# Kernel optimization log

Hardware: AMD Instinct MI355X
Metric: run time of the kernel (lower is better)

The kernel has to match this reference:

```python
import jax, jax.numpy as jnp
import numpy as np

LN_EPS = 1e-5


def setup_inputs() -> dict:
    key = jax.random.key(0)
    ks = jax.random.split(key, 6)
    B, I, H = 16384, 512, 512
    x = jax.random.normal(ks[0], (B, I), dtype=jnp.float32)
    h_prev = jax.random.normal(ks[1], (B, H), dtype=jnp.float32)
    c_prev = jax.random.normal(ks[2], (B, H), dtype=jnp.float32)
    # packed gate weights in i|f|g|o order (equivalent to 8 separate matmuls)
    W_i = jax.random.normal(ks[3], (I, 4 * H), dtype=jnp.float32) * (1.0 / np.sqrt(I))
    W_h = jax.random.normal(ks[4], (H, 4 * H), dtype=jnp.float32) * (1.0 / np.sqrt(H))
    # biases: b_i=0, b_f=1, b_g=0, b_o=0 as in the torch module
    b = jnp.concatenate([jnp.zeros(H), jnp.ones(H), jnp.zeros(H), jnp.zeros(H)]).astype(jnp.float32)
    ln_weight = jnp.ones((H,), dtype=jnp.float32)
    ln_bias = jnp.zeros((H,), dtype=jnp.float32)
    return {"x": x, "h_prev": h_prev, "c_prev": c_prev, "W_i": W_i, "W_h": W_h,
            "b": b, "ln_weight": ln_weight, "ln_bias": ln_bias}


def layer_norm(h, w, bias):
    mu = jnp.mean(h, axis=-1, keepdims=True)
    var = jnp.var(h, axis=-1, keepdims=True)
    return (h - mu) * jax.lax.rsqrt(var + LN_EPS) * w + bias


def reference(x, h_prev, c_prev, W_i, W_h, b, ln_weight, ln_bias):
    H = h_prev.shape[-1]
    # two fused GEMMs covering all 4 gates: [B, 4H]
    gates = x @ W_i + h_prev @ W_h + b
    i, f, g, o = jnp.split(gates, 4, axis=-1)
    i = jax.nn.sigmoid(i)
    f = jax.nn.sigmoid(f)
    g = jnp.tanh(g)
    o = jax.nn.sigmoid(o)
    c = f * c_prev + i * g
    h = o * jnp.tanh(c)
    h = layer_norm(h, ln_weight, ln_bias)
    return (h, c)
```

## Files before the change

### kernel.cpp

```cpp
#include <hip/hip_runtime.h>
#include <cstdint>
#include <cstddef>

typedef unsigned short ushort_t;
typedef __attribute__((ext_vector_type(8))) short bf16x8;
typedef __attribute__((ext_vector_type(4))) float f32x4;

#define MROWS 16384
#define KDIM  1024
#define NDIM  2048
#define HDIM  512

static __device__ __forceinline__ unsigned short f2bf(float f) {
    unsigned int u = __float_as_uint(f);
    u += 0x7fffu + ((u >> 16) & 1u);
    return (unsigned short)(u >> 16);
}

static __device__ __forceinline__ float sigmoid_f(float x) {
    return 1.0f / (1.0f + __expf(-x));
}
static __device__ __forceinline__ float tanh_f(float x) {
    float t = __expf(2.0f * x);
    return 1.0f - 2.0f / (t + 1.0f);
}

__global__ __launch_bounds__(256) void pack_ab(const float* __restrict__ x,
                                               const float* __restrict__ hp,
                                               const float* __restrict__ Wi,
                                               const float* __restrict__ Wh,
                                               ushort_t* __restrict__ A,
                                               ushort_t* __restrict__ Bt) {
    __shared__ ushort_t sm[64][72];
    const int tid = threadIdx.x;
    if (blockIdx.x < 8192) {
        int t = blockIdx.x * 256 + tid;
        int row = t >> 7;
        int kc = (t & 127) << 3;
        const float* src = (kc < 512) ? (x + (size_t)row * 512 + kc)
                                      : (hp + (size_t)row * 512 + (kc - 512));
        float4 v0 = ((const float4*)src)[0];
        float4 v1 = ((const float4*)src)[1];
        ushort_t o[8] __attribute__((aligned(16)));
        o[0] = f2bf(v0.x); o[1] = f2bf(v0.y); o[2] = f2bf(v0.z); o[3] = f2bf(v0.w);
        o[4] = f2bf(v1.x); o[5] = f2bf(v1.y); o[6] = f2bf(v1.z); o[7] = f2bf(v1.w);
        *((uint4*)(A + (size_t)row * KDIM + kc)) = *((const uint4*)o);
    } else {
        int b2 = blockIdx.x - 8192;
        int kt = b2 >> 5;
        int ct = b2 & 31;
        const float* W = (kt < 8) ? (Wi + (size_t)(kt * 64) * NDIM)
                                  : (Wh + (size_t)((kt - 8) * 64) * NDIM);
        int c0 = (tid & 15) * 4;
        int r0 = tid >> 4;
#pragma unroll
        for (int r = 0; r < 4; ++r) {
            int krow = r * 16 + r0;
            float4 v = *((const float4*)(W + (size_t)krow * NDIM + ct * 64 + c0));
            sm[krow][c0 + 0] = f2bf(v.x);
            sm[krow][c0 + 1] = f2bf(v.y);
            sm[krow][c0 + 2] = f2bf(v.z);
            sm[krow][c0 + 3] = f2bf(v.w);
        }
        __syncthreads();
        int g = (ct * 64) >> 9;
        int h0 = ct * 64 - g * 512;
#pragma unroll
        for (int q = tid; q < 512; q += 256) {
            int cc = q >> 3;
            int kc = (q & 7) * 8;
            ushort_t o[8] __attribute__((aligned(16)));
#pragma unroll
            for (int j = 0; j < 8; ++j) o[j] = sm[kc + j][cc];
            int np = 4 * (h0 + cc) + g;
            *((uint4*)(Bt + (size_t)np * KDIM + kt * 64 + kc)) = *((const uint4*)o);
        }
    }
}

__global__ __launch_bounds__(256, 4) void gemm_cell(const ushort_t* __restrict__ A,
                                                    const ushort_t* __restrict__ Bt,
                                                    const float* __restrict__ b,
                                                    const float* __restrict__ c_prev,
                                                    float* __restrict__ h_out,
                                                    float* __restrict__ c_out) {
    __shared__ float smem_f[6144];
    ushort_t* Als = (ushort_t*)smem_f;
    ushort_t* Bls = Als + 128 * 64;

    const int tid  = threadIdx.x;
    const int w    = tid >> 6;
    const int lane = tid & 63;
    int bid = blockIdx.x;
    int lid = (bid >> 3) + (bid & 7) * 512;
    const int m0 = (lid >> 5) * 128;
    const int n0 = (lid & 31) * 64;
    const int wm = (w >> 1) * 64;
    const int wn = (w & 1) * 32;
    const int lr   = lane & 15;
    const int quad = lane >> 4;
    const int sw   = lr & 7;

    f32x4 zero = {0.f, 0.f, 0.f, 0.f};
    f32x4 acc[4][2];
#pragma unroll
    for (int i = 0; i < 4; ++i)
#pragma unroll
        for (int j = 0; j < 2; ++j) acc[i][j] = zero;

    for (int kt = 0; kt < KDIM / 64; ++kt) {
#pragma unroll
        for (int r = 0; r < 4; ++r) {
            int c = r * 256 + tid;
            int trow = c >> 3;
            int chg = (c & 7) ^ (trow & 7);
            const ushort_t* ga = A + (size_t)(m0 + trow) * KDIM + kt * 64 + chg * 8;
            __builtin_amdgcn_global_load_lds(
                (const __attribute__((address_space(1))) void*)ga,
                (__attribute__((address_space(3))) void*)((char*)Als + c * 16),
                16, 0, 0);
        }
#pragma unroll
        for (int r = 0; r < 2; ++r) {
            int c = r * 256 + tid;
            int trow = c >> 3;
            int chg = (c & 7) ^ (trow & 7);
            const ushort_t* gb = Bt + (size_t)(n0 + trow) * KDIM + kt * 64 + chg * 8;
            __builtin_amdgcn_global_load_lds(
                (const __attribute__((address_space(1))) void*)gb,
                (__attribute__((address_space(3))) void*)((char*)Bls + c * 16),
                16, 0, 0);
        }
        __syncthreads();

#pragma unroll
        for (int kk = 0; kk < 2; ++kk) {
            bf16x8 af[4], bf[2];
            int ch = kk * 4 + quad;
#pragma unroll
            for (int t2 = 0; t2 < 4; ++t2) {
                int ra = wm + t2 * 16 + lr;
                af[t2] = *((const bf16x8*)(Als + (ra * 8 + (ch ^ sw)) * 8));
            }
#pragma unroll
            for (int t2 = 0; t2 < 2; ++t2) {
                int rb = wn + t2 * 16 + lr;
                bf[t2] = *((const bf16x8*)(Bls + (rb * 8 + (ch ^ sw)) * 8));
            }
#pragma unroll
            for (int tm = 0; tm < 4; ++tm)
#pragma unroll
                for (int tn = 0; tn < 2; ++tn)
                    acc[tm][tn] = __builtin_amdgcn_mfma_f32_16x16x32_bf16(
                        af[tm], bf[tn], acc[tm][tn], 0, 0, 0);
        }
        __syncthreads();
    }

    float* scr = smem_f + w * 1024;
    const int hg0 = ((n0 + wn) >> 2) + ((lane & 1) << 2);
    const float4 bi4 = *((const float4*)(b + hg0));
    const float4 bf4 = *((const float4*)(b + 512 + hg0));
    const float4 bg4 = *((const float4*)(b + 1024 + hg0));
    const float4 bo4 = *((const float4*)(b + 1536 + hg0));
    const int rr = lane >> 1;

#pragma unroll
    for (int chunk = 0; chunk < 2; ++chunk) {
#pragma unroll
        for (int tm2 = 0; tm2 < 2; ++tm2) {
            int tm = chunk * 2 + tm2;
#pragma unroll
            for (int tn = 0; tn < 2; ++tn) {
                int c = tn * 16 + lr;
#pragma unroll
                for (int rg = 0; rg < 4; ++rg) {
                    int r = tm2 * 16 + quad * 4 + rg;
                    int blk = (c >> 2) ^ (r & 7);
                    scr[r * 32 + blk * 4 + (c & 3)] = acc[tm][tn][rg];
                }
            }
        }
        float4 gv[4];
#pragma unroll
        for (int j = 0; j < 4; ++j) {
            int hg_l = ((lane & 1) << 2) + j;
            int blk = hg_l ^ (rr & 7);
            gv[j] = *((const float4*)(scr + rr * 32 + blk * 4));
        }
        int grow = m0 + wm + chunk * 32 + rr;
        float4 cp = *((const float4*)(c_prev + (size_t)grow * HDIM + hg0));
        float cn[4], hv[4];
        {
            float iv, fv, g2, ov;
            iv = sigmoid_f(gv[0].x + bi4.x); fv = sigmoid_f(gv[0].y + bf4.x);
            g2 = tanh_f(gv[0].z + bg4.x);    ov = sigmoid_f(gv[0].w + bo4.x);
            cn[0] = fv * cp.x + iv * g2;     hv[0] = ov * tanh_f(cn[0]);
            iv = sigmoid_f(gv[1].x + bi4.y); fv = sigmoid_f(gv[1].y + bf4.y);
            g2 = tanh_f(gv[1].z + bg4.y);    ov = sigmoid_f(gv[1].w + bo4.y);
            cn[1] = fv * cp.y + iv * g2;     hv[1] = ov * tanh_f(cn[1]);
            iv = sigmoid_f(gv[2].x + bi4.z); fv = sigmoid_f(gv[2].y + bf4.z);
            g2 = tanh_f(gv[2].z + bg4.z);    ov = sigmoid_f(gv[2].w + bo4.z);
            cn[2] = fv * cp.z + iv * g2;     hv[2] = ov * tanh_f(cn[2]);
            iv = sigmoid_f(gv[3].x + bi4.w); fv = sigmoid_f(gv[3].y + bf4.w);
            g2 = tanh_f(gv[3].z + bg4.w);    ov = sigmoid_f(gv[3].w + bo4.w);
            cn[3] = fv * cp.w + iv * g2;     hv[3] = ov * tanh_f(cn[3]);
        }
        float4 cno = {cn[0], cn[1], cn[2], cn[3]};
        float4 hvo = {hv[0], hv[1], hv[2], hv[3]};
        *((float4*)(c_out + (size_t)grow * HDIM + hg0)) = cno;
        *((float4*)(h_out + (size_t)grow * HDIM + hg0)) = hvo;
    }
}

__global__ __launch_bounds__(256) void ln_kernel(float* __restrict__ h,
                                                 const float* __restrict__ lw,
                                                 const float* __restrict__ lb) {
    int w = threadIdx.x >> 6;
    int lane = threadIdx.x & 63;
    int row = blockIdx.x * 4 + w;
    float* p = h + (size_t)row * HDIM + lane * 8;
    float4 a = ((const float4*)p)[0];
    float4 c = ((const float4*)p)[1];
    float s  = a.x + a.y + a.z + a.w + c.x + c.y + c.z + c.w;
    float ss = a.x * a.x + a.y * a.y + a.z * a.z + a.w * a.w +
               c.x * c.x + c.y * c.y + c.z * c.z + c.w * c.w;
#pragma unroll
    for (int off = 32; off > 0; off >>= 1) {
        s  += __shfl_xor(s, off);
        ss += __shfl_xor(ss, off);
    }
    float mu = s * (1.0f / 512.0f);
    float var = ss * (1.0f / 512.0f) - mu * mu;
    float rstd = rsqrtf(var + 1e-5f);
    const float* wp = lw + lane * 8;
    const float* bp = lb + lane * 8;
    float4 w0 = ((const float4*)wp)[0];
    float4 w1 = ((const float4*)wp)[1];
    float4 b0 = ((const float4*)bp)[0];
    float4 b1 = ((const float4*)bp)[1];
    a.x = (a.x - mu) * rstd * w0.x + b0.x;
    a.y = (a.y - mu) * rstd * w0.y + b0.y;
    a.z = (a.z - mu) * rstd * w0.z + b0.z;
    a.w = (a.w - mu) * rstd * w0.w + b0.w;
    c.x = (c.x - mu) * rstd * w1.x + b1.x;
    c.y = (c.y - mu) * rstd * w1.y + b1.y;
    c.z = (c.z - mu) * rstd * w1.z + b1.z;
    c.w = (c.w - mu) * rstd * w1.w + b1.w;
    ((float4*)p)[0] = a;
    ((float4*)p)[1] = c;
}

extern "C" void kernel_launch(void* const* d_in, const int* in_sizes, int n_in,
                              void* d_out, int out_size, void* d_ws, size_t ws_size,
                              hipStream_t stream) {
    const float* x      = (const float*)d_in[0];
    const float* h_prev = (const float*)d_in[1];
    const float* c_prev = (const float*)d_in[2];
    const float* W_i    = (const float*)d_in[3];
    const float* W_h    = (const float*)d_in[4];
    const float* b      = (const float*)d_in[5];
    const float* ln_w   = (const float*)d_in[6];
    const float* ln_b   = (const float*)d_in[7];

    float* h_out = (float*)d_out;
    float* c_out = h_out + (size_t)MROWS * HDIM;

    ushort_t* A  = (ushort_t*)d_ws;
    ushort_t* Bt = A + (size_t)MROWS * KDIM;

    pack_ab<<<8192 + 512, 256, 0, stream>>>(x, h_prev, W_i, W_h, A, Bt);
    gemm_cell<<<4096, 256, 0, stream>>>(A, Bt, b, c_prev, h_out, c_out);
    ln_kernel<<<MROWS / 4, 256, 0, stream>>>(h_out, ln_w, ln_b);
}
```

Before: 257.0 us.

## Enlarge GEMM block tile to 256x64 with 64x64 warp tiles

Doubles the M dimension of each workgroup tile from 128 to 256 rows and gives each wave a 64x64 output tile (4x4 MFMA fragments) instead of 64x32, halving the grid to 2048 blocks. This raises arithmetic intensity per LDS load and B-tile reuse, reducing global and LDS traffic per FLOP. The epilogue is reworked to transpose 16-row slices through shared memory with a new swizzle. In exchange it uses more registers (64 accumulator floats) and more LDS (40KB), which may lower occupancy under the launch bound of 4.

```diff
diff --git a/kernel.cpp b/kernel.cpp
--- a/kernel.cpp
+++ b/kernel.cpp
@@ -84,33 +84,32 @@
                                                     const float* __restrict__ c_prev,
                                                     float* __restrict__ h_out,
                                                     float* __restrict__ c_out) {
-    __shared__ float smem_f[6144];
+    __shared__ float smem_f[10240];
     ushort_t* Als = (ushort_t*)smem_f;
-    ushort_t* Bls = Als + 128 * 64;
+    ushort_t* Bls = Als + 256 * 64;
 
     const int tid  = threadIdx.x;
     const int w    = tid >> 6;
     const int lane = tid & 63;
     int bid = blockIdx.x;
-    int lid = (bid >> 3) + (bid & 7) * 512;
-    const int m0 = (lid >> 5) * 128;
+    int lid = (bid >> 3) + (bid & 7) * 256;
+    const int m0 = (lid >> 5) * 256;
     const int n0 = (lid & 31) * 64;
-    const int wm = (w >> 1) * 64;
-    const int wn = (w & 1) * 32;
+    const int wm = w * 64;
     const int lr   = lane & 15;
     const int quad = lane >> 4;
     const int sw   = lr & 7;
 
     f32x4 zero = {0.f, 0.f, 0.f, 0.f};
-    f32x4 acc[4][2];
+    f32x4 acc[4][4];
 #pragma unroll
     for (int i = 0; i < 4; ++i)
 #pragma unroll
-        for (int j = 0; j < 2; ++j) acc[i][j] = zero;
+        for (int j = 0; j < 4; ++j) acc[i][j] = zero;
 
     for (int kt = 0; kt < KDIM / 64; ++kt) {
 #pragma unroll
-        for (int r = 0; r < 4; ++r) {
+        for (int r = 0; r < 8; ++r) {
             int c = r * 256 + tid;
             int trow = c >> 3;
             int chg = (c & 7) ^ (trow & 7);
@@ -135,7 +134,7 @@
 
 #pragma unroll
         for (int kk = 0; kk < 2; ++kk) {
-            bf16x8 af[4], bf[2];
+            bf16x8 af[4], bfr[4];
             int ch = kk * 4 + quad;
 #pragma unroll
             for (int t2 = 0; t2 < 4; ++t2) {
@@ -143,68 +142,62 @@
                 af[t2] = *((const bf16x8*)(Als + (ra * 8 + (ch ^ sw)) * 8));
             }
 #pragma unroll
-            for (int t2 = 0; t2 < 2; ++t2) {
-                int rb = wn + t2 * 16 + lr;
-                bf[t2] = *((const bf16x8*)(Bls + (rb * 8 + (ch ^ sw)) * 8));
+            for (int t2 = 0; t2 < 4; ++t2) {
+                int rb = t2 * 16 + lr;
+                bfr[t2] = *((const bf16x8*)(Bls + (rb * 8 + (ch ^ sw)) * 8));
             }
 #pragma unroll
             for (int tm = 0; tm < 4; ++tm)
 #pragma unroll
-                for (int tn = 0; tn < 2; ++tn)
+                for (int tn = 0; tn < 4; ++tn)
                     acc[tm][tn] = __builtin_amdgcn_mfma_f32_16x16x32_bf16(
-                        af[tm], bf[tn], acc[tm][tn], 0, 0, 0);
+                        af[tm], bfr[tn], acc[tm][tn], 0, 0, 0);
         }
         __syncthreads();
     }
 
     float* scr = smem_f + w * 1024;
-    const int hg0 = ((n0 + wn) >> 2) + ((lane & 1) << 2);
+    const int rr = lane >> 2;
+    const int hg0 = (n0 >> 2) + (lane & 3) * 4;
     const float4 bi4 = *((const float4*)(b + hg0));
-    const float4 bf4 = *((const float4*)(b + 512 + hg0));
-    const float4 bg4 = *((const float4*)(b + 1024 + hg0));
-    const float4 bo4 = *((const float4*)(b + 1536 + hg0));
-    const int rr = lane >> 1;
-
-#pragma unroll
-    for (int chunk = 0; chunk < 2; ++chunk) {
-#pragma unroll
-        for (int tm2 = 0; tm2 < 2; ++tm2) {
-            int tm = chunk * 2 + tm2;
-#pragma unroll
-            for (int tn = 0; tn < 2; ++tn) {
-                int c = tn * 16 + lr;
-#pragma unroll
-                for (int rg = 0; rg < 4; ++rg) {
-                    int r = tm2 * 16 + quad * 4 + rg;
-                    int blk = (c >> 2) ^ (r & 7);
-                    scr[r * 32 + blk * 4 + (c & 3)] = acc[tm][tn][rg];
-                }
+    const float4 bff = *((const float4*)(b + 512 + hg0));
+    const float4 bgg = *((const float4*)(b + 1024 + hg0));
+    const float4 boo = *((const float4*)(b + 1536 + hg0));
+    const float bi[4] = {bi4.x, bi4.y, bi4.z, bi4.w};
+    const float bfv[4] = {bff.x, bff.y, bff.z, bff.w};
+    const float bg[4] = {bgg.x, bgg.y, bgg.z, bgg.w};
+    const float bo[4] = {boo.x, boo.y, boo.z, boo.w};
+
+#pragma unroll
+    for (int tm = 0; tm < 4; ++tm) {
+#pragma unroll
+        for (int tn = 0; tn < 4; ++tn) {
+            int c = tn * 16 + lr;
+#pragma unroll
+            for (int rg = 0; rg < 4; ++rg) {
+                int r = quad * 4 + rg;
+                int blk = (c >> 2) ^ r;
+                scr[r * 64 + blk * 4 + (c & 3)] = acc[tm][tn][rg];
             }
         }
         float4 gv[4];
 #pragma unroll
         for (int j = 0; j < 4; ++j) {
-            int hg_l = ((lane & 1) << 2) + j;
-            int blk = hg_l ^ (rr & 7);
-            gv[j] = *((const float4*)(scr + rr * 32 + blk * 4));
-        }
-        int grow = m0 + wm + chunk * 32 + rr;
-        float4 cp = *((const float4*)(c_prev + (size_t)grow * HDIM + hg0));
+            int cb = (lane & 3) * 4 + j;
+            gv[j] = *((const float4*)(scr + rr * 64 + (cb ^ rr) * 4));
+        }
+        int grow = m0 + wm + tm * 16 + rr;
+        float4 cp4 = *((const float4*)(c_prev + (size_t)grow * HDIM + hg0));
+        const float cpv[4] = {cp4.x, cp4.y, cp4.z, cp4.w};
         float cn[4], hv[4];
-        {
-            float iv, fv, g2, ov;
-            iv = sigmoid_f(gv[0].x + bi4.x); fv = sigmoid_f(gv[0].y + bf4.x);
-            g2 = tanh_f(gv[0].z + bg4.x);    ov = sigmoid_f(gv[0].w + bo4.x);
-            cn[0] = fv * cp.x + iv * g2;     hv[0] = ov * tanh_f(cn[0]);
-            iv = sigmoid_f(gv[1].x + bi4.y); fv = sigmoid_f(gv[1].y + bf4.y);
-            g2 = tanh_f(gv[1].z + bg4.y);    ov = sigmoid_f(gv[1].w + bo4.y);
-            cn[1] = fv * cp.y + iv * g2;     hv[1] = ov * tanh_f(cn[1]);
-            iv = sigmoid_f(gv[2].x + bi4.z); fv = sigmoid_f(gv[2].y + bf4.z);
-            g2 = tanh_f(gv[2].z + bg4.z);    ov = sigmoid_f(gv[2].w + bo4.z);
-            cn[2] = fv * cp.z + iv * g2;     hv[2] = ov * tanh_f(cn[2]);
-            iv = sigmoid_f(gv[3].x + bi4.w); fv = sigmoid_f(gv[3].y + bf4.w);
-            g2 = tanh_f(gv[3].z + bg4.w);    ov = sigmoid_f(gv[3].w + bo4.w);
-            cn[3] = fv * cp.w + iv * g2;     hv[3] = ov * tanh_f(cn[3]);
+#pragma unroll
+        for (int j = 0; j < 4; ++j) {
+            float iv = sigmoid_f(gv[j].x + bi[j]);
+            float fv = sigmoid_f(gv[j].y + bfv[j]);
+            float g2 = tanh_f(gv[j].z + bg[j]);
+            float ov = sigmoid_f(gv[j].w + bo[j]);
+            cn[j] = fv * cpv[j] + iv * g2;
+            hv[j] = ov * tanh_f(cn[j]);
         }
         float4 cno = {cn[0], cn[1], cn[2], cn[3]};
         float4 hvo = {hv[0], hv[1], hv[2], hv[3]};
@@ -270,6 +263,6 @@
     ushort_t* Bt = A + (size_t)MROWS * KDIM;
 
     pack_ab<<<8192 + 512, 256, 0, stream>>>(x, h_prev, W_i, W_h, A, Bt);
-    gemm_cell<<<4096, 256, 0, stream>>>(A, Bt, b, c_prev, h_out, c_out);
+    gemm_cell<<<2048, 256, 0, stream>>>(A, Bt, b, c_prev, h_out, c_out);
     ln_kernel<<<MROWS / 4, 256, 0, stream>>>(h_out, ln_w, ln_b);
 }
```

After: 254.8 us. Within noise of the previous version (-0.8%).
